# Kernel tuning notes

Measured on AMD Instinct MI355X. Metric: run time of the kernel, lower is better.

The kernel has to match this reference:

```python
import jax, jax.numpy as jnp
import numpy as np

N_NODES = 50000
N_EDGES = 400000
MUL_IN = 32      # input node irreps: 32x0e
MUL_OUT = 64     # target irreps: 64x0e+64x1o+64x2e+64x3o
DENOM = 8.0

# component-normalized real spherical harmonics, l = 1, 2, 3, on unit vectors
_S3, _S5, _S7, _S15, _S42, _S70, _S105 = (np.sqrt(v).astype(np.float32) for v in (3., 5., 7., 15., 42., 70., 105.))

def spherical_harmonics_123(vec):
    # vec: [E, 3]; normalize=True semantics
    r = jnp.linalg.norm(vec, axis=-1, keepdims=True)
    u = vec / jnp.maximum(r, 1e-12)
    x, y, z = u[..., 0], u[..., 1], u[..., 2]
    x2, y2, z2 = x * x, y * y, z * z
    sh1 = jnp.stack([_S3 * x, _S3 * y, _S3 * z], axis=-1)                      # [E, 3]
    sh2 = jnp.stack([
        _S15 * x * y,
        _S15 * y * z,
        0.5 * _S5 * (3.0 * z2 - 1.0),
        _S15 * x * z,
        0.5 * _S15 * (x2 - y2),
    ], axis=-1)                                                                # [E, 5]
    sh3 = jnp.stack([
        0.25 * _S70 * y * (3.0 * x2 - y2),
        _S105 * x * y * z,
        0.25 * _S42 * y * (5.0 * z2 - 1.0),
        0.5 * _S7 * z * (5.0 * z2 - 3.0),
        0.25 * _S42 * x * (5.0 * z2 - 1.0),
        0.5 * _S105 * z * (x2 - y2),
        0.25 * _S70 * x * (x2 - 3.0 * y2),
    ], axis=-1)                                                                # [E, 7]
    return sh1, sh2, sh3


def setup_inputs() -> dict:
    key = jax.random.key(0)
    ks = jax.random.split(key, 9)
    return {
        "positions": jax.random.normal(ks[0], (N_NODES, 3), jnp.float32),
        "node_feats": jax.random.normal(ks[1], (N_NODES, MUL_IN), jnp.float32),
        "W0": jax.random.normal(ks[2], (MUL_IN, MUL_OUT), jnp.float32),
        "W1": jax.random.normal(ks[3], (MUL_IN, MUL_OUT), jnp.float32),
        "W2": jax.random.normal(ks[4], (MUL_IN, MUL_OUT), jnp.float32),
        "W3": jax.random.normal(ks[5], (MUL_IN, MUL_OUT), jnp.float32),
        "Wsc": jax.random.normal(ks[6], (MUL_IN, MUL_OUT), jnp.float32),
        "senders": jax.random.randint(ks[7], (N_EDGES,), 0, N_NODES),
        "receivers": jax.random.randint(ks[8], (N_EDGES,), 0, N_NODES),
    }


def reference(positions, node_feats, W0, W1, W2, W3, Wsc, senders, receivers):
    E = senders.shape[0]
    # ---- update_edge_fn: gather senders, SH of edge vectors, 0e x l tensor product ----
    sf = node_feats[senders]                                      # [E, 32] (32x0e)
    rel = positions[receivers] - positions[senders]               # [E, 3]
    sh1, sh2, sh3 = spherical_harmonics_123(rel)
    # tensor product 32x0e (x) (1o+2e+3o): CG for 0e x l -> l is identity
    tp1 = (sf[:, :, None] * sh1[:, None, :]).reshape(E, -1)       # [E, 32*3]
    tp2 = (sf[:, :, None] * sh2[:, None, :]).reshape(E, -1)       # [E, 32*5]
    tp3 = (sf[:, :, None] * sh3[:, None, :]).reshape(E, -1)       # [E, 32*7]
    messages = jnp.concatenate([sf, tp1, tp2, tp3], axis=-1)      # [E, 512]: 32x0e+32x1o+32x2e+32x3o

    # ---- GraphNetwork aggregation: sum messages at receivers ----
    agg = jax.ops.segment_sum(messages, receivers, num_segments=N_NODES)  # [N, 512]
    nf = agg / DENOM

    # ---- update_node_fn: e3nn Linear per-l (path-normalized by 1/sqrt(fan_in)) ----
    scale = 1.0 / np.sqrt(MUL_IN).astype(np.float32)
    s = nf[:, :MUL_IN]                                            # [N, 32]
    v1 = nf[:, MUL_IN:MUL_IN * 4].reshape(-1, MUL_IN, 3)
    v2 = nf[:, MUL_IN * 4:MUL_IN * 9].reshape(-1, MUL_IN, 5)
    v3 = nf[:, MUL_IN * 9:].reshape(-1, MUL_IN, 7)

    out0 = (s @ W0) * scale                                       # [N, 64]
    out1 = jnp.einsum('nmi,mt->nti', v1, W1) * scale              # [N, 64, 3]
    out2 = jnp.einsum('nmi,mt->nti', v2, W2) * scale              # [N, 64, 5]
    out3 = jnp.einsum('nmi,mt->nti', v3, W3) * scale              # [N, 64, 7]

    # shortcut Linear from 32x0e (force_irreps_out: only the 0e block is nonzero)
    out0 = out0 + (node_feats @ Wsc) * scale

    N = node_feats.shape[0]
    return jnp.concatenate(
        [out0, out1.reshape(N, -1), out2.reshape(N, -1), out3.reshape(N, -1)], axis=-1
    )  # [N, 1024]
```

## Files before the change

### kernel.cpp

```cpp
#include <hip/hip_runtime.h>

#define NN 50000
#define NE 400000
#define SCAN_NB 196

__global__ void k_hist(const int* __restrict__ rcv, int* __restrict__ cnt){
  int e = blockIdx.x*256 + threadIdx.x;
  if (e < NE) atomicAdd(&cnt[rcv[e]], 1);
}

__global__ void k_scanA(const int* __restrict__ cnt, int* __restrict__ bsum){
  __shared__ int sh[256];
  int i = blockIdx.x*256 + threadIdx.x;
  int v = (i < NN) ? cnt[i] : 0;
  sh[threadIdx.x] = v; __syncthreads();
  for (int off=128; off>0; off>>=1){
    if (threadIdx.x < off) sh[threadIdx.x] += sh[threadIdx.x+off];
    __syncthreads();
  }
  if (threadIdx.x==0) bsum[blockIdx.x] = sh[0];
}

__global__ void k_scanB(int* __restrict__ bsum){
  __shared__ int sh[256];
  int t = threadIdx.x;
  int v = (t < SCAN_NB) ? bsum[t] : 0;
  sh[t] = v; __syncthreads();
  for (int off=1; off<256; off<<=1){
    int x = (t>=off)? sh[t-off] : 0;
    __syncthreads();
    sh[t] += x;
    __syncthreads();
  }
  if (t < SCAN_NB) bsum[t] = sh[t] - v;
}

__global__ void k_scanC(const int* __restrict__ cnt, const int* __restrict__ bsum,
                        int* __restrict__ offs, int* __restrict__ cursor){
  __shared__ int sh[256];
  int t = threadIdx.x;
  int i = blockIdx.x*256 + t;
  int v = (i < NN) ? cnt[i] : 0;
  sh[t] = v; __syncthreads();
  for (int off=1; off<256; off<<=1){
    int x = (t>=off)? sh[t-off] : 0;
    __syncthreads();
    sh[t] += x;
    __syncthreads();
  }
  int excl = sh[t] - v + bsum[blockIdx.x];
  if (i < NN){ offs[i] = excl; cursor[i] = excl; }
}

__global__ void k_scatter(const int* __restrict__ rcv, const int* __restrict__ snd,
                          int* __restrict__ cursor, int* __restrict__ csr_snd){
  int e = blockIdx.x*256 + threadIdx.x;
  if (e < NE){
    int p = atomicAdd(&cursor[rcv[e]], 1);
    csr_snd[p] = snd[e];
  }
}

__global__ __launch_bounds__(1024) void k_edge(
    const float* __restrict__ pos, const float* __restrict__ feat,
    const float* __restrict__ W0, const float* __restrict__ W1,
    const float* __restrict__ W2, const float* __restrict__ W3,
    const float* __restrict__ Wsc,
    const int* __restrict__ offs, const int* __restrict__ cnt,
    const int* __restrict__ csr_snd, float* __restrict__ out)
{
  __shared__ float Wl[5][2048];
  __shared__ __align__(16) float sm[16][512];
  __shared__ int slist[16][32];

  const int tid = threadIdx.x;
  {
    const float* src[5] = {W0,W1,W2,W3,Wsc};
    #pragma unroll
    for (int w=0; w<5; ++w)
      for (int i=tid; i<2048; i+=1024)
        Wl[w][i] = src[w][i];
  }
  __syncthreads();

  const int wv = tid>>6, lane = tid&63;
  const int ml = lane&31, hh = lane>>5;
  const int n = blockIdx.x*16 + wv;
  const float pnx=pos[n*3], pny=pos[n*3+1], pnz=pos[n*3+2];
  const int start = offs[n], deg = cnt[n];
  const int nch = (deg+31)>>5;

  float acc[8];
  #pragma unroll
  for (int j=0;j<8;++j) acc[j]=0.f;

  const float SC3=1.7320508f, SC5=2.236068f, SC7=2.6457513f, SC15=3.8729833f,
              SC42=6.4807407f, SC70=8.3666003f, SC105=10.246951f;

  for (int c=0; c<nch; ++c){
    const int base = c<<5;
    int cn = deg - base; cn = (cn>32)?32:cn;
    if (lane < cn){
      int s = csr_snd[start+base+lane];
      float rx = pnx - pos[s*3];
      float ry = pny - pos[s*3+1];
      float rz = pnz - pos[s*3+2];
      float r = sqrtf(rx*rx+ry*ry+rz*rz);
      float inv = 1.0f/fmaxf(r,1e-12f);
      float x=rx*inv, y=ry*inv, z=rz*inv;
      float x2=x*x, y2=y*y, z2=z*z;
      float s1=SC3*x, s2=SC3*y, s3=SC3*z;
      float s4=SC15*x*y, s5=SC15*y*z, s6=0.5f*SC5*(3.f*z2-1.f), s7=SC15*x*z;
      float s8=0.5f*SC15*(x2-y2);
      float s9 =0.25f*SC70*y*(3.f*x2-y2);
      float s10=SC105*x*y*z;
      float s11=0.25f*SC42*y*(5.f*z2-1.f);
      float s12=0.5f*SC7*z*(5.f*z2-3.f);
      float s13=0.25f*SC42*x*(5.f*z2-1.f);
      float s14=0.5f*SC105*z*(x2-y2);
      float s15=0.25f*SC70*x*(x2-3.f*y2);
      float4* wp = (float4*)&sm[wv][lane*16];
      wp[0] = make_float4(1.0f,s1,s2,s3);
      wp[1] = make_float4(s4,s5,s6,s7);
      wp[2] = make_float4(s8,s9,s10,s11);
      wp[3] = make_float4(s12,s13,s14,s15);
      slist[wv][lane] = s;
    }
    asm volatile("s_waitcnt lgkmcnt(0)" ::: "memory");
    #pragma unroll 4
    for (int it=0; it<cn; ++it){
      int s = __builtin_amdgcn_readfirstlane(slist[wv][it]);
      float f = feat[(size_t)s*32 + ml];
      const float4* rp = (const float4*)&sm[wv][it*16 + hh*8];
      float4 q0=rp[0], q1=rp[1];
      acc[0]+=f*q0.x; acc[1]+=f*q0.y; acc[2]+=f*q0.z; acc[3]+=f*q0.w;
      acc[4]+=f*q1.x; acc[5]+=f*q1.y; acc[6]+=f*q1.z; acc[7]+=f*q1.w;
    }
    asm volatile("" ::: "memory");
  }

  {
    float4* ap = (float4*)&sm[wv][ml*16 + hh*8];
    ap[0] = make_float4(acc[0],acc[1],acc[2],acc[3]);
    ap[1] = make_float4(acc[4],acc[5],acc[6],acc[7]);
  }
  asm volatile("s_waitcnt lgkmcnt(0)" ::: "memory");

  float oa[16];
  #pragma unroll
  for (int k=0;k<16;++k) oa[k]=0.f;
  float osc = 0.f;
  const float4* fs4 = (const float4*)(feat + (size_t)n*32);

  #pragma unroll 2
  for (int g=0; g<8; ++g){
    float4 fsv = fs4[g];
    #pragma unroll
    for (int mm=0; mm<4; ++mm){
      const int m = g*4+mm;
      const float fsm = (mm==0)?fsv.x:(mm==1)?fsv.y:(mm==2)?fsv.z:fsv.w;
      const float4* Ap = (const float4*)&sm[wv][m*16];
      float4 a0=Ap[0], a1=Ap[1], a2=Ap[2], a3=Ap[3];
      float w0=Wl[0][m*64+lane], w1=Wl[1][m*64+lane], w2=Wl[2][m*64+lane],
            w3=Wl[3][m*64+lane], w4=Wl[4][m*64+lane];
      oa[0] += a0.x*w0;
      oa[1] += a0.y*w1; oa[2] += a0.z*w1; oa[3] += a0.w*w1;
      oa[4] += a1.x*w2; oa[5] += a1.y*w2; oa[6] += a1.z*w2;
      oa[7] += a1.w*w2; oa[8] += a2.x*w2;
      oa[9] += a2.y*w3; oa[10]+= a2.z*w3; oa[11]+= a2.w*w3;
      oa[12]+= a3.x*w3; oa[13]+= a3.y*w3; oa[14]+= a3.z*w3; oa[15]+= a3.w*w3;
      osc += fsm*w4;
    }
  }

  const float S = 0.17677669529663687f;
  const float S8 = S*0.125f;
  float* o = out + (size_t)n*1024;
  o[lane] = oa[0]*S8 + osc*S;
  #pragma unroll
  for (int i=0;i<3;++i) o[64  + lane*3 + i] = oa[1+i]*S8;
  #pragma unroll
  for (int i=0;i<5;++i) o[256 + lane*5 + i] = oa[4+i]*S8;
  #pragma unroll
  for (int i=0;i<7;++i) o[576 + lane*7 + i] = oa[9+i]*S8;
}

extern "C" void kernel_launch(void* const* d_in, const int* in_sizes, int n_in,
                              void* d_out, int out_size, void* d_ws, size_t ws_size,
                              hipStream_t stream) {
  const float* pos  = (const float*)d_in[0];
  const float* feat = (const float*)d_in[1];
  const float* W0   = (const float*)d_in[2];
  const float* W1   = (const float*)d_in[3];
  const float* W2   = (const float*)d_in[4];
  const float* W3   = (const float*)d_in[5];
  const float* Wsc  = (const float*)d_in[6];
  const int*  snd   = (const int*)d_in[7];
  const int*  rcv   = (const int*)d_in[8];
  float* out = (float*)d_out;

  int* ws      = (int*)d_ws;
  int* cnt     = ws;
  int* offs    = ws + 50000;
  int* cursor  = ws + 100000;
  int* bsum    = ws + 150000;
  int* csr_snd = ws + 150272;

  hipMemsetAsync(cnt, 0, NN*sizeof(int), stream);
  k_hist   <<<(NE+255)/256, 256, 0, stream>>>(rcv, cnt);
  k_scanA  <<<SCAN_NB, 256, 0, stream>>>(cnt, bsum);
  k_scanB  <<<1, 256, 0, stream>>>(bsum);
  k_scanC  <<<SCAN_NB, 256, 0, stream>>>(cnt, bsum, offs, cursor);
  k_scatter<<<(NE+255)/256, 256, 0, stream>>>(rcv, snd, cursor, csr_snd);
  k_edge   <<<3125, 1024, 0, stream>>>(pos, feat, W0, W1, W2, W3, Wsc,
                                       offs, cnt, csr_snd, out);
}
```

Measured before the change: 444.4 us.

## Split fused edge kernel into aggregation and transform kernels with packed weights

The single 1024-thread kernel, which staged all five weight matrices (40KB) plus per-wave scratch in LDS, is split into two kernels. k_aggr gathers over 64-edge chunks and passes sender indices through readlane instead of LDS. It writes the per-node 512-float aggregate to a global buffer. k_xform reloads that buffer and applies the linear layers, reading W0..W3 interleaved as float4 from global memory or cache. The aim is to cut LDS footprint and raise occupancy. The cost is an extra ~100MB round trip through global memory and extra launches.

```diff
diff --git a/kernel.cpp b/kernel.cpp
--- a/kernel.cpp
+++ b/kernel.cpp
@@ -61,34 +61,26 @@
   }
 }
 
-__global__ __launch_bounds__(1024) void k_edge(
+__global__ void k_prepW(const float* __restrict__ W0, const float* __restrict__ W1,
+                        const float* __restrict__ W2, const float* __restrict__ W3,
+                        float4* __restrict__ Wp){
+  int i = blockIdx.x*256 + threadIdx.x;
+  if (i < 2048) Wp[i] = make_float4(W0[i], W1[i], W2[i], W3[i]);
+}
+
+__global__ __launch_bounds__(256) void k_aggr(
     const float* __restrict__ pos, const float* __restrict__ feat,
-    const float* __restrict__ W0, const float* __restrict__ W1,
-    const float* __restrict__ W2, const float* __restrict__ W3,
-    const float* __restrict__ Wsc,
     const int* __restrict__ offs, const int* __restrict__ cnt,
-    const int* __restrict__ csr_snd, float* __restrict__ out)
+    const int* __restrict__ csr_snd, float4* __restrict__ A4)
 {
-  __shared__ float Wl[5][2048];
-  __shared__ __align__(16) float sm[16][512];
-  __shared__ int slist[16][32];
-
-  const int tid = threadIdx.x;
-  {
-    const float* src[5] = {W0,W1,W2,W3,Wsc};
-    #pragma unroll
-    for (int w=0; w<5; ++w)
-      for (int i=tid; i<2048; i+=1024)
-        Wl[w][i] = src[w][i];
-  }
-  __syncthreads();
-
-  const int wv = tid>>6, lane = tid&63;
+  __shared__ __align__(16) float smS[4][64][16];
+
+  const int tid = threadIdx.x, wv = tid>>6, lane = tid&63;
   const int ml = lane&31, hh = lane>>5;
-  const int n = blockIdx.x*16 + wv;
+  const int n = blockIdx.x*4 + wv;
   const float pnx=pos[n*3], pny=pos[n*3+1], pnz=pos[n*3+2];
   const int start = offs[n], deg = cnt[n];
-  const int nch = (deg+31)>>5;
+  const int nch = (deg+63)>>6;
 
   float acc[8];
   #pragma unroll
@@ -98,13 +90,14 @@
               SC42=6.4807407f, SC70=8.3666003f, SC105=10.246951f;
 
   for (int c=0; c<nch; ++c){
-    const int base = c<<5;
-    int cn = deg - base; cn = (cn>32)?32:cn;
+    const int base = c<<6;
+    int cn = deg - base; cn = (cn>64)?64:cn;
+    int sE = 0;
     if (lane < cn){
-      int s = csr_snd[start+base+lane];
-      float rx = pnx - pos[s*3];
-      float ry = pny - pos[s*3+1];
-      float rz = pnz - pos[s*3+2];
+      sE = csr_snd[start+base+lane];
+      float rx = pnx - pos[sE*3];
+      float ry = pny - pos[sE*3+1];
+      float rz = pnz - pos[sE*3+2];
       float r = sqrtf(rx*rx+ry*ry+rz*rz);
       float inv = 1.0f/fmaxf(r,1e-12f);
       float x=rx*inv, y=ry*inv, z=rz*inv;
@@ -119,19 +112,18 @@
       float s13=0.25f*SC42*x*(5.f*z2-1.f);
       float s14=0.5f*SC105*z*(x2-y2);
       float s15=0.25f*SC70*x*(x2-3.f*y2);
-      float4* wp = (float4*)&sm[wv][lane*16];
+      float4* wp = (float4*)&smS[wv][lane][0];
       wp[0] = make_float4(1.0f,s1,s2,s3);
       wp[1] = make_float4(s4,s5,s6,s7);
       wp[2] = make_float4(s8,s9,s10,s11);
       wp[3] = make_float4(s12,s13,s14,s15);
-      slist[wv][lane] = s;
     }
     asm volatile("s_waitcnt lgkmcnt(0)" ::: "memory");
-    #pragma unroll 4
+    #pragma unroll 8
     for (int it=0; it<cn; ++it){
-      int s = __builtin_amdgcn_readfirstlane(slist[wv][it]);
+      int s = __builtin_amdgcn_readlane(sE, it);
       float f = feat[(size_t)s*32 + ml];
-      const float4* rp = (const float4*)&sm[wv][it*16 + hh*8];
+      const float4* rp = (const float4*)&smS[wv][it][hh*8];
       float4 q0=rp[0], q1=rp[1];
       acc[0]+=f*q0.x; acc[1]+=f*q0.y; acc[2]+=f*q0.z; acc[3]+=f*q0.w;
       acc[4]+=f*q1.x; acc[5]+=f*q1.y; acc[6]+=f*q1.z; acc[7]+=f*q1.w;
@@ -139,38 +131,52 @@
     asm volatile("" ::: "memory");
   }
 
-  {
-    float4* ap = (float4*)&sm[wv][ml*16 + hh*8];
-    ap[0] = make_float4(acc[0],acc[1],acc[2],acc[3]);
-    ap[1] = make_float4(acc[4],acc[5],acc[6],acc[7]);
-  }
+  float4* dst = A4 + (size_t)n*128 + ml*4 + hh*2;
+  dst[0] = make_float4(acc[0],acc[1],acc[2],acc[3]);
+  dst[1] = make_float4(acc[4],acc[5],acc[6],acc[7]);
+}
+
+__global__ __launch_bounds__(256) void k_xform(
+    const float* __restrict__ feat, const float4* __restrict__ A4,
+    const float4* __restrict__ Wp, const float* __restrict__ Wsc,
+    float* __restrict__ out)
+{
+  __shared__ __align__(16) float4 smA[4][128];
+
+  const int tid = threadIdx.x, wv = tid>>6, lane = tid&63;
+  const int n = blockIdx.x*4 + wv;
+
+  const float4* Ap = A4 + (size_t)n*128;
+  smA[wv][lane]    = Ap[lane];
+  smA[wv][lane+64] = Ap[lane+64];
   asm volatile("s_waitcnt lgkmcnt(0)" ::: "memory");
+
+  float4 F[8];
+  const float4* f4 = (const float4*)(feat + (size_t)n*32);
+  #pragma unroll
+  for (int g=0; g<8; ++g) F[g] = f4[g];
 
   float oa[16];
   #pragma unroll
   for (int k=0;k<16;++k) oa[k]=0.f;
   float osc = 0.f;
-  const float4* fs4 = (const float4*)(feat + (size_t)n*32);
-
-  #pragma unroll 2
-  for (int g=0; g<8; ++g){
-    float4 fsv = fs4[g];
-    #pragma unroll
-    for (int mm=0; mm<4; ++mm){
-      const int m = g*4+mm;
-      const float fsm = (mm==0)?fsv.x:(mm==1)?fsv.y:(mm==2)?fsv.z:fsv.w;
-      const float4* Ap = (const float4*)&sm[wv][m*16];
-      float4 a0=Ap[0], a1=Ap[1], a2=Ap[2], a3=Ap[3];
-      float w0=Wl[0][m*64+lane], w1=Wl[1][m*64+lane], w2=Wl[2][m*64+lane],
-            w3=Wl[3][m*64+lane], w4=Wl[4][m*64+lane];
-      oa[0] += a0.x*w0;
-      oa[1] += a0.y*w1; oa[2] += a0.z*w1; oa[3] += a0.w*w1;
-      oa[4] += a1.x*w2; oa[5] += a1.y*w2; oa[6] += a1.z*w2;
-      oa[7] += a1.w*w2; oa[8] += a2.x*w2;
-      oa[9] += a2.y*w3; oa[10]+= a2.z*w3; oa[11]+= a2.w*w3;
-      oa[12]+= a3.x*w3; oa[13]+= a3.y*w3; oa[14]+= a3.z*w3; oa[15]+= a3.w*w3;
-      osc += fsm*w4;
-    }
+
+  #pragma unroll 4
+  for (int m=0; m<32; ++m){
+    float4 wq = Wp[m*64 + lane];
+    float  w4 = Wsc[m*64 + lane];
+    float4 a0 = smA[wv][m*4+0];
+    float4 a1 = smA[wv][m*4+1];
+    float4 a2 = smA[wv][m*4+2];
+    float4 a3 = smA[wv][m*4+3];
+    const float fsm = ((const float*)&F[m>>2])[m&3];
+    oa[0] += a0.x*wq.x;
+    oa[1] += a0.y*wq.y; oa[2] += a0.z*wq.y; oa[3] += a0.w*wq.y;
+    oa[4] += a1.x*wq.z; oa[5] += a1.y*wq.z; oa[6] += a1.z*wq.z;
+    oa[7] += a1.w*wq.z; oa[8] += a2.x*wq.z;
+    oa[9] += a2.y*wq.w; oa[10]+= a2.z*wq.w; oa[11]+= a2.w*wq.w;
+    oa[12]+= a3.x*wq.w; oa[13]+= a3.y*wq.w; oa[14]+= a3.z*wq.w; oa[15]+= a3.w*wq.w;
+    osc += fsm*w4;
   }
 
   const float S = 0.17677669529663687f;
@@ -205,6 +211,8 @@
   int* cursor  = ws + 100000;
   int* bsum    = ws + 150000;
   int* csr_snd = ws + 150272;
+  float4* Wp   = (float4*)(ws + 550272);
+  float4* A4   = (float4*)(ws + 558464);
 
   hipMemsetAsync(cnt, 0, NN*sizeof(int), stream);
   k_hist   <<<(NE+255)/256, 256, 0, stream>>>(rcv, cnt);
@@ -212,6 +220,7 @@
   k_scanB  <<<1, 256, 0, stream>>>(bsum);
   k_scanC  <<<SCAN_NB, 256, 0, stream>>>(cnt, bsum, offs, cursor);
   k_scatter<<<(NE+255)/256, 256, 0, stream>>>(rcv, snd, cursor, csr_snd);
-  k_edge   <<<3125, 1024, 0, stream>>>(pos, feat, W0, W1, W2, W3, Wsc,
-                                       offs, cnt, csr_snd, out);
-}
+  k_prepW  <<<8, 256, 0, stream>>>(W0, W1, W2, W3, Wp);
+  k_aggr   <<<12500, 256, 0, stream>>>(pos, feat, offs, cnt, csr_snd, A4);
+  k_xform  <<<12500, 256, 0, stream>>>(feat, A4, Wp, Wsc, out);
+}
```

Measured after the change: 524.7 us. +18.1%, slower.
